# Optimization experiments

Hardware: AMD Instinct MI355X
Metric: run time of the kernel (lower is better)

The kernel has to match this reference:

```python
import jax, jax.numpy as jnp
import numpy as np

DIM, HEAD, SR = 512, 8, 2
LN_EPS = 1e-5


def _layernorm(x, g, b):
    mu = jnp.mean(x, axis=-1, keepdims=True)
    var = jnp.mean((x - mu) ** 2, axis=-1, keepdims=True)
    return (x - mu) * jax.lax.rsqrt(var + LN_EPS) * g + b


def setup_inputs() -> dict:
    key = jax.random.key(0)
    ks = jax.random.split(key, 16)
    B, N, C = 8, 4096, DIM
    s = 1.0 / np.sqrt(C)
    inp = {
        "x": jax.random.normal(ks[0], (B, N, C), jnp.float32),
        "context": jax.random.normal(ks[1], (B, N, C), jnp.float32),
        # Linear weights in torch layout [out, in]
        "Wq": jax.random.normal(ks[2], (C, C), jnp.float32) * s,
        "bq": jnp.zeros((C,), jnp.float32),
        "Wk": jax.random.normal(ks[3], (C, C), jnp.float32) * s,
        "bk": jnp.zeros((C,), jnp.float32),
        "Wv": jax.random.normal(ks[4], (C, C), jnp.float32) * s,
        "bv": jnp.zeros((C,), jnp.float32),
        "Wp": jax.random.normal(ks[5], (C, C), jnp.float32) * s,
        "bp": jnp.zeros((C,), jnp.float32),
        # spatial-reduction convs, OIHW, kernel=stride=SR
        "Wsrk": jax.random.normal(ks[6], (C, C, SR, SR), jnp.float32) * s / SR,
        "bsrk": jnp.zeros((C,), jnp.float32),
        "Wsrv": jax.random.normal(ks[7], (C, C, SR, SR), jnp.float32) * s / SR,
        "bsrv": jnp.zeros((C,), jnp.float32),
        "gk": jnp.ones((C,), jnp.float32),
        "bek": jnp.zeros((C,), jnp.float32),
        "gv": jnp.ones((C,), jnp.float32),
        "bev": jnp.zeros((C,), jnp.float32),
        "H": 64,
        "W": 64,
    }
    return inp


def reference(x, context, Wq, bq, Wk, bk, Wv, bv, Wp, bp,
              Wsrk, bsrk, Wsrv, bsrv, gk, bek, gv, bev, H, W):
    B, N, C = x.shape
    h, d = HEAD, C // HEAD
    scale = d ** (-0.5)

    # spatial reduction on context (sr_ratio > 1 branch)
    ctx = jnp.transpose(context, (0, 2, 1)).reshape(B, C, H, W)  # [B,C,H,W]
    dn = (("NCHW", "OIHW", "NCHW"))

    def sr(kernel, bias):
        y = jax.lax.conv_general_dilated(ctx, kernel, (SR, SR), "VALID",
                                         dimension_numbers=dn)
        y = y + bias[None, :, None, None]
        return jnp.transpose(y.reshape(B, C, -1), (0, 2, 1))  # [B,M,C]

    ctx_k = _layernorm(sr(Wsrk, bsrk), gk, bek)
    ctx_v = _layernorm(sr(Wsrv, bsrv), gv, bev)

    q = (x @ Wq.T + bq).reshape(B, N, h, d)          # [B,N,h,d]
    k = (ctx_k @ Wk.T + bk).reshape(B, -1, h, d)     # [B,M,h,d]
    v = (ctx_v @ Wv.T + bv).reshape(B, -1, h, d)     # [B,M,h,d]

    attn = jnp.einsum("bnhd,bmhd->bhnm", q, k) * scale
    attn = jax.nn.softmax(attn, axis=-1)
    out = jnp.einsum("bhnm,bmhd->bnhd", attn, v).reshape(B, N, C)
    return out @ Wp.T + bp
```

## Files before the change

### kernel.cpp

```cpp
#include <hip/hip_runtime.h>
#include <hip/hip_bf16.h>

typedef float f32x4 __attribute__((ext_vector_type(4)));
typedef short bf16x8 __attribute__((ext_vector_type(8)));
typedef unsigned short ushort_t;

__device__ __forceinline__ ushort_t f2bf(float f) {
    union { float f; unsigned u; } v; v.f = f;
    unsigned r = v.u + 0x7fffu + ((v.u >> 16) & 1u);
    return (ushort_t)(r >> 16);
}
__device__ __forceinline__ float bf2f(ushort_t h) {
    union { unsigned u; float f; } v; v.u = ((unsigned)h) << 16;
    return v.f;
}

__device__ __forceinline__ void async16(ushort_t* lds, const ushort_t* g) {
    __builtin_amdgcn_global_load_lds(
        (const __attribute__((address_space(1))) unsigned int*)g,
        (__attribute__((address_space(3))) unsigned int*)lds, 16, 0, 0);
}

__global__ __launch_bounds__(256) void cast2_bf16_kernel(const float* __restrict__ s0,
                                                         const float* __restrict__ s1,
                                                         ushort_t* __restrict__ dst) {
    long idx = (long)blockIdx.x * 256 + threadIdx.x;
    int sel = (int)(idx >> 21);
    const float* s = sel ? s1 : s0;
    long off = (idx & 2097151) * 8;
    float4 a = *(const float4*)(s + off);
    float4 b = *(const float4*)(s + off + 4);
    ushort_t o[8];
    o[0]=f2bf(a.x); o[1]=f2bf(a.y); o[2]=f2bf(a.z); o[3]=f2bf(a.w);
    o[4]=f2bf(b.x); o[5]=f2bf(b.y); o[6]=f2bf(b.z); o[7]=f2bf(b.w);
    *(bf16x8*)(dst + (long)sel * 16777216 + off) = *(bf16x8*)o;
}

__global__ __launch_bounds__(256) void cast_w4_kernel(const float* __restrict__ s0,
                                                      const float* __restrict__ s1,
                                                      const float* __restrict__ s2,
                                                      const float* __restrict__ s3,
                                                      ushort_t* __restrict__ dst) {
    long idx = (long)blockIdx.x * 256 + threadIdx.x;
    int sel = (int)(idx >> 15);
    const float* s = sel == 0 ? s0 : sel == 1 ? s1 : sel == 2 ? s2 : s3;
    long off = (idx & 32767) * 8;
    float4 a = *(const float4*)(s + off);
    float4 b = *(const float4*)(s + off + 4);
    ushort_t o[8];
    o[0]=f2bf(a.x); o[1]=f2bf(a.y); o[2]=f2bf(a.z); o[3]=f2bf(a.w);
    o[4]=f2bf(b.x); o[5]=f2bf(b.y); o[6]=f2bf(b.z); o[7]=f2bf(b.w);
    *(bf16x8*)(dst + (long)sel * 262144 + off) = *(bf16x8*)o;
}

__global__ __launch_bounds__(256) void pack_wsr2_kernel(const float* __restrict__ w0,
                                                        const float* __restrict__ w1,
                                                        ushort_t* __restrict__ out) {
    int idx = blockIdx.x * 256 + threadIdx.x;
    int sel = idx >> 18;
    const float* w = sel ? w1 : w0;
    int li = idx & 262143;
    int c = li >> 9, ci = li & 511;
    float4 t = *(const float4*)(w + c * 2048 + ci * 4);
    ushort_t* ob = out + sel * 1048576 + c * 2048 + ci;
    ob[0]    = f2bf(t.x);
    ob[512]  = f2bf(t.y);
    ob[1024] = f2bf(t.z);
    ob[1536] = f2bf(t.w);
}

struct GemmJob {
    const ushort_t* A;
    const ushort_t* Bw;
    const float* bias;
    void* C;
    int omode;
    int M;
    int K;
    int gather;
    float oscale;
};

__global__ __launch_bounds__(256) void gemm_multi(GemmJob j0, GemmJob j1, GemmJob j2,
                                                  int nb0, int nb1) {
    __shared__ __align__(16) ushort_t As[128][64];
    __shared__ __align__(16) ushort_t Bs[128][64];
    const int bid = blockIdx.x;
    GemmJob j;
    int local;
    if (bid < nb0)            { j = j0; local = bid; }
    else if (bid < nb0 + nb1) { j = j1; local = bid - nb0; }
    else                      { j = j2; local = bid - nb0 - nb1; }

    const int tid  = threadIdx.x;
    const int row0 = (((local & 7) | ((local >> 5) << 3))) * 128;
    const int col0 = ((local >> 3) & 3) * 128;
    const int wave = tid >> 6, lane = tid & 63;
    const int rw = wave >> 1, cw = wave & 1;
    const int l15 = lane & 15, l4 = lane >> 4;
    const int srow = wave * 8 + (lane >> 3);
    const int sc8  = (lane & 7) * 8;
    const int K = j.K;

    f32x4 acc[4][4] = {};

    for (int k0 = 0; k0 < K; k0 += 64) {
        __syncthreads();
#pragma unroll
        for (int p = 0; p < 4; ++p) {
            int r = p * 32 + srow;
            const ushort_t* ga;
            if (j.gather) {
                int gr = row0 + r;
                int b = gr >> 10, m = gr & 1023;
                int mh = m >> 5, mw = m & 31;
                int tap = k0 >> 9;
                int kh = tap >> 1, kw = tap & 1;
                ga = j.A + ((long)(b * 4096 + (2 * mh + kh) * 64 + (2 * mw + kw))) * 512
                         + (k0 & 511) + sc8;
            } else {
                ga = j.A + (long)(row0 + r) * K + k0 + sc8;
            }
            async16(&As[p * 32 + wave * 8][0], ga);
            async16(&Bs[p * 32 + wave * 8][0],
                    j.Bw + (long)(col0 + r) * K + k0 + sc8);
        }
        __syncthreads();
#pragma unroll
        for (int ks = 0; ks < 2; ++ks) {
            bf16x8 af[4], bfr[4];
#pragma unroll
            for (int i = 0; i < 4; ++i)
                af[i] = *(const bf16x8*)&As[rw * 64 + i * 16 + l15][ks * 32 + l4 * 8];
#pragma unroll
            for (int jj = 0; jj < 4; ++jj)
                bfr[jj] = *(const bf16x8*)&Bs[cw * 64 + jj * 16 + l15][ks * 32 + l4 * 8];
#pragma unroll
            for (int i = 0; i < 4; ++i)
#pragma unroll
                for (int jj = 0; jj < 4; ++jj)
                    acc[i][jj] = __builtin_amdgcn_mfma_f32_16x16x32_bf16(af[i], bfr[jj],
                                                                         acc[i][jj], 0, 0, 0);
        }
    }
#pragma unroll
    for (int i = 0; i < 4; ++i) {
#pragma unroll
        for (int jj = 0; jj < 4; ++jj) {
            int col = col0 + cw * 64 + jj * 16 + l15;
            float bv = j.bias[col];
#pragma unroll
            for (int r = 0; r < 4; ++r) {
                int row = row0 + rw * 64 + i * 16 + l4 * 4 + r;
                float v = (acc[i][jj][r] + bv) * j.oscale;
                if (j.omode == 0) {
                    ((ushort_t*)j.C)[(long)row * 512 + col] = f2bf(v);
                } else if (j.omode == 1) {
                    ((float*)j.C)[(long)row * 512 + col] = v;
                } else {
                    int b = row >> 10, m = row & 1023;
                    int hh = col >> 6, dd = col & 63;
                    ((ushort_t*)j.C)[(((long)(b * 8 + hh) * 64 + dd) << 10) + m] = f2bf(v);
                }
            }
        }
    }
}

__global__ __launch_bounds__(256) void ln_kernel(ushort_t* __restrict__ data,
                                                 const float* __restrict__ g0,
                                                 const float* __restrict__ be0,
                                                 const float* __restrict__ g1,
                                                 const float* __restrict__ be1) {
    int wave = threadIdx.x >> 6, lane = threadIdx.x & 63;
    long row = (long)blockIdx.x * 4 + wave;
    const float* g  = row < 8192 ? g0 : g1;
    const float* be = row < 8192 ? be0 : be1;
    ushort_t* p = data + row * 512 + lane * 8;
    bf16x8 raw = *(bf16x8*)p;
    ushort_t* rp = (ushort_t*)&raw;
    float v[8], s = 0.f, s2 = 0.f;
#pragma unroll
    for (int j = 0; j < 8; ++j) { v[j] = bf2f(rp[j]); s += v[j]; s2 += v[j] * v[j]; }
#pragma unroll
    for (int d = 1; d < 64; d <<= 1) { s += __shfl_xor(s, d); s2 += __shfl_xor(s2, d); }
    float mu  = s * (1.f / 512.f);
    float var = s2 * (1.f / 512.f) - mu * mu;
    float rs  = rsqrtf(var + 1e-5f);
    ushort_t o[8];
#pragma unroll
    for (int j = 0; j < 8; ++j) {
        int c = lane * 8 + j;
        o[j] = f2bf((v[j] - mu) * rs * g[c] + be[c]);
    }
    *(bf16x8*)p = *(bf16x8*)o;
}

__global__ __launch_bounds__(256, 3) void attn_kernel(const ushort_t* __restrict__ q,
                                                      const ushort_t* __restrict__ k,
                                                      const ushort_t* __restrict__ vt,
                                                      ushort_t* __restrict__ o) {
    __shared__ __align__(16) ushort_t Ks[128][72];
    __shared__ __align__(16) ushort_t Vs[64][136];

    const int tid = threadIdx.x;
    const int wave = tid >> 6, lane = tid & 63;
    const int l15 = lane & 15, l4 = lane >> 4;
    const int n0 = blockIdx.x * 128;
    const int hh = blockIdx.y;
    const int b  = blockIdx.z;

    bf16x8 bq[2][2];
#pragma unroll
    for (int nb = 0; nb < 2; ++nb)
#pragma unroll
        for (int ks = 0; ks < 2; ++ks)
            bq[nb][ks] = *(const bf16x8*)(
                q + (long)(b * 4096 + n0 + wave * 32 + nb * 16 + l15) * 512
                  + hh * 64 + ks * 32 + l4 * 8);

    f32x4 oacc[2][4] = {};
    f32x4 lacc[2] = {};
    union { bf16x8 v8; unsigned u[4]; } ones;
    ones.u[0] = ones.u[1] = ones.u[2] = ones.u[3] = 0x3F803F80u;

    for (int c = 0; c < 8; ++c) {
        const int m0 = c * 128;
        __syncthreads();
#pragma unroll
        for (int p = 0; p < 4; ++p) {
            int qi = p * 256 + tid;
            int r = qi >> 3, c8 = (qi & 7) * 8;
            bf16x8 v = *(const bf16x8*)(k + (((long)(b * 1024 + m0 + r) * 8 + hh) << 6) + c8);
            *(bf16x8*)&Ks[r][c8] = v;
        }
#pragma unroll
        for (int p = 0; p < 4; ++p) {
            int qi = p * 256 + tid;
            int dd = qi >> 4, c8 = (qi & 15) * 8;
            bf16x8 v = *(const bf16x8*)(vt + (((long)(b * 8 + hh) * 64 + dd) << 10) + m0 + c8);
            *(bf16x8*)&Vs[dd][c8] = v;
        }
        __syncthreads();

        f32x4 s[2][8] = {};
        __builtin_amdgcn_s_setprio(1);
#pragma unroll
        for (int ks = 0; ks < 2; ++ks) {
#pragma unroll
            for (int i = 0; i < 8; ++i) {
                bf16x8 ak = *(const bf16x8*)&Ks[i * 16 + l15][ks * 32 + l4 * 8];
                s[0][i] = __builtin_amdgcn_mfma_f32_16x16x32_bf16(ak, bq[0][ks], s[0][i], 0, 0, 0);
                s[1][i] = __builtin_amdgcn_mfma_f32_16x16x32_bf16(ak, bq[1][ks], s[1][i], 0, 0, 0);
            }
        }
        __builtin_amdgcn_s_setprio(0);

        unsigned pk[2][8][2];
#pragma unroll
        for (int nb = 0; nb < 2; ++nb)
#pragma unroll
            for (int i = 0; i < 8; ++i) {
                float e0 = __builtin_amdgcn_exp2f(s[nb][i][0]);
                float e1 = __builtin_amdgcn_exp2f(s[nb][i][1]);
                float e2 = __builtin_amdgcn_exp2f(s[nb][i][2]);
                float e3 = __builtin_amdgcn_exp2f(s[nb][i][3]);
                asm("v_cvt_pk_bf16_f32 %0, %1, %2" : "=v"(pk[nb][i][0]) : "v"(e0), "v"(e1));
                asm("v_cvt_pk_bf16_f32 %0, %1, %2" : "=v"(pk[nb][i][1]) : "v"(e2), "v"(e3));
            }

        __builtin_amdgcn_s_setprio(1);
#pragma unroll
        for (int mb = 0; mb < 4; ++mb) {
            union { bf16x8 v8; unsigned long long h[2]; } bfr[4];
#pragma unroll
            for (int db = 0; db < 4; ++db) {
                bfr[db].h[0] = *(const unsigned long long*)&Vs[db * 16 + l15][mb * 32 + l4 * 4];
                bfr[db].h[1] = *(const unsigned long long*)&Vs[db * 16 + l15][mb * 32 + 16 + l4 * 4];
            }
#pragma unroll
            for (int nb = 0; nb < 2; ++nb) {
                union { bf16x8 v8; unsigned u32v[4]; } af;
                af.u32v[0] = pk[nb][2 * mb][0];
                af.u32v[1] = pk[nb][2 * mb][1];
                af.u32v[2] = pk[nb][2 * mb + 1][0];
                af.u32v[3] = pk[nb][2 * mb + 1][1];
                lacc[nb] = __builtin_amdgcn_mfma_f32_16x16x32_bf16(af.v8, ones.v8,
                                                                   lacc[nb], 0, 0, 0);
#pragma unroll
                for (int db = 0; db < 4; ++db)
                    oacc[nb][db] = __builtin_amdgcn_mfma_f32_16x16x32_bf16(af.v8, bfr[db].v8,
                                                                           oacc[nb][db], 0, 0, 0);
            }
        }
        __builtin_amdgcn_s_setprio(0);
    }

#pragma unroll
    for (int nb = 0; nb < 2; ++nb)
#pragma unroll
        for (int r = 0; r < 4; ++r) {
            float inv = 1.f / lacc[nb][r];
            int n = wave * 32 + nb * 16 + l4 * 4 + r;
#pragma unroll
            for (int db = 0; db < 4; ++db) {
                int dd = db * 16 + l15;
                o[((long)(b * 4096 + n0 + n)) * 512 + hh * 64 + dd] = f2bf(oacc[nb][db][r] * inv);
            }
        }
}

extern "C" void kernel_launch(void* const* d_in, const int* in_sizes, int n_in,
                              void* d_out, int out_size, void* d_ws, size_t ws_size,
                              hipStream_t stream) {
    const float* x    = (const float*)d_in[0];
    const float* ctx  = (const float*)d_in[1];
    const float* Wq   = (const float*)d_in[2];
    const float* bq   = (const float*)d_in[3];
    const float* Wk   = (const float*)d_in[4];
    const float* bk   = (const float*)d_in[5];
    const float* Wv   = (const float*)d_in[6];
    const float* bv   = (const float*)d_in[7];
    const float* Wp   = (const float*)d_in[8];
    const float* bp   = (const float*)d_in[9];
    const float* Wsrk = (const float*)d_in[10];
    const float* bsrk = (const float*)d_in[11];
    const float* Wsrv = (const float*)d_in[12];
    const float* bsrv = (const float*)d_in[13];
    const float* gk   = (const float*)d_in[14];
    const float* bek  = (const float*)d_in[15];
    const float* gv   = (const float*)d_in[16];
    const float* bev  = (const float*)d_in[17];

    ushort_t* x_bf    = (ushort_t*)d_ws;
    ushort_t* ctx_bf  = x_bf    + 16777216;
    ushort_t* q_bf    = ctx_bf  + 16777216;
    ushort_t* at_bf   = q_bf    + 16777216;
    ushort_t* k_bf    = at_bf   + 16777216;
    ushort_t* vt_bf   = k_bf    + 4194304;
    ushort_t* convk   = vt_bf   + 4194304;
    ushort_t* convv   = convk   + 4194304;
    ushort_t* wq_bf   = convv   + 4194304;
    ushort_t* wk_bf   = wq_bf   + 262144;
    ushort_t* wv_bf   = wk_bf   + 262144;
    ushort_t* wp_bf   = wv_bf   + 262144;
    ushort_t* wsrk_p  = wp_bf   + 262144;
    ushort_t* wsrv_p  = wsrk_p  + 1048576;

    const float EC = 0.18033688011112042f;

    cast2_bf16_kernel<<<16384, 256, 0, stream>>>(x, ctx, x_bf);
    cast_w4_kernel<<<512, 256, 0, stream>>>(Wq, Wk, Wv, Wp, wq_bf);
    pack_wsr2_kernel<<<2048, 256, 0, stream>>>(Wsrk, Wsrv, wsrk_p);

    GemmJob jck = { ctx_bf, wsrk_p, bsrk, convk, 0, 8192,  2048, 1, 1.0f };
    GemmJob jcv = { ctx_bf, wsrv_p, bsrv, convv, 0, 8192,  2048, 1, 1.0f };
    GemmJob jq  = { x_bf,  wq_bf,  bq,   q_bf,  0, 32768, 512,  0, EC };
    gemm_multi<<<1536, 256, 0, stream>>>(jck, jcv, jq, 256, 256);

    ln_kernel<<<4096, 256, 0, stream>>>(convk, gk, bek, gv, bev);

    GemmJob jk  = { convk, wk_bf, bk, k_bf,  0, 8192, 512, 0, 1.0f };
    GemmJob jv  = { convv, wv_bf, bv, vt_bf, 2, 8192, 512, 0, 1.0f };
    gemm_multi<<<512, 256, 0, stream>>>(jk, jv, jv, 256, 256);

    attn_kernel<<<dim3(32, 8, 8), 256, 0, stream>>>(q_bf, k_bf, vt_bf, at_bf);

    GemmJob jo  = { at_bf, wp_bf, bp, d_out, 1, 32768, 512, 0, 1.0f };
    gemm_multi<<<1024, 256, 0, stream>>>(jo, jo, jo, 1024, 0);
}
```

Before: 435.3 us.

## Fuse fp32-to-bf16 activation cast into GEMM A-tile loads and merge weight prep kernels

Drops the separate cast kernel for x and context. The first GEMM launch now reads fp32 activations directly and converts them to bf16 while staging the A tile into LDS, which removes a full write and re-read of two large bf16 copies. The weight cast and conv-weight pack kernels are also merged into one launch. In exchange, the fp32 A path uses synchronous register loads instead of async global-to-LDS copies. The conv gather now reads each context element four times in fp32 rather than bf16, which doubles the bytes per reread.

```diff
diff --git a/kernel.cpp b/kernel.cpp
--- a/kernel.cpp
+++ b/kernel.cpp
@@ -21,56 +21,43 @@
         (__attribute__((address_space(3))) unsigned int*)lds, 16, 0, 0);
 }
 
-__global__ __launch_bounds__(256) void cast2_bf16_kernel(const float* __restrict__ s0,
-                                                         const float* __restrict__ s1,
-                                                         ushort_t* __restrict__ dst) {
-    long idx = (long)blockIdx.x * 256 + threadIdx.x;
-    int sel = (int)(idx >> 21);
-    const float* s = sel ? s1 : s0;
-    long off = (idx & 2097151) * 8;
-    float4 a = *(const float4*)(s + off);
-    float4 b = *(const float4*)(s + off + 4);
-    ushort_t o[8];
-    o[0]=f2bf(a.x); o[1]=f2bf(a.y); o[2]=f2bf(a.z); o[3]=f2bf(a.w);
-    o[4]=f2bf(b.x); o[5]=f2bf(b.y); o[6]=f2bf(b.z); o[7]=f2bf(b.w);
-    *(bf16x8*)(dst + (long)sel * 16777216 + off) = *(bf16x8*)o;
-}
-
-__global__ __launch_bounds__(256) void cast_w4_kernel(const float* __restrict__ s0,
-                                                      const float* __restrict__ s1,
-                                                      const float* __restrict__ s2,
-                                                      const float* __restrict__ s3,
-                                                      ushort_t* __restrict__ dst) {
-    long idx = (long)blockIdx.x * 256 + threadIdx.x;
-    int sel = (int)(idx >> 15);
-    const float* s = sel == 0 ? s0 : sel == 1 ? s1 : sel == 2 ? s2 : s3;
-    long off = (idx & 32767) * 8;
-    float4 a = *(const float4*)(s + off);
-    float4 b = *(const float4*)(s + off + 4);
-    ushort_t o[8];
-    o[0]=f2bf(a.x); o[1]=f2bf(a.y); o[2]=f2bf(a.z); o[3]=f2bf(a.w);
-    o[4]=f2bf(b.x); o[5]=f2bf(b.y); o[6]=f2bf(b.z); o[7]=f2bf(b.w);
-    *(bf16x8*)(dst + (long)sel * 262144 + off) = *(bf16x8*)o;
-}
-
-__global__ __launch_bounds__(256) void pack_wsr2_kernel(const float* __restrict__ w0,
-                                                        const float* __restrict__ w1,
-                                                        ushort_t* __restrict__ out) {
-    int idx = blockIdx.x * 256 + threadIdx.x;
-    int sel = idx >> 18;
-    const float* w = sel ? w1 : w0;
-    int li = idx & 262143;
-    int c = li >> 9, ci = li & 511;
-    float4 t = *(const float4*)(w + c * 2048 + ci * 4);
-    ushort_t* ob = out + sel * 1048576 + c * 2048 + ci;
-    ob[0]    = f2bf(t.x);
-    ob[512]  = f2bf(t.y);
-    ob[1024] = f2bf(t.z);
-    ob[1536] = f2bf(t.w);
+__global__ __launch_bounds__(256) void prep_w_kernel(const float* __restrict__ Wq,
+                                                     const float* __restrict__ Wk,
+                                                     const float* __restrict__ Wv,
+                                                     const float* __restrict__ Wp,
+                                                     ushort_t* __restrict__ wdst,
+                                                     const float* __restrict__ w0,
+                                                     const float* __restrict__ w1,
+                                                     ushort_t* __restrict__ pout) {
+    int bid = blockIdx.x;
+    if (bid < 512) {
+        long idx = (long)bid * 256 + threadIdx.x;
+        int sel = (int)(idx >> 15);
+        const float* s = sel == 0 ? Wq : sel == 1 ? Wk : sel == 2 ? Wv : Wp;
+        long off = (idx & 32767) * 8;
+        float4 a = *(const float4*)(s + off);
+        float4 b = *(const float4*)(s + off + 4);
+        ushort_t o[8];
+        o[0]=f2bf(a.x); o[1]=f2bf(a.y); o[2]=f2bf(a.z); o[3]=f2bf(a.w);
+        o[4]=f2bf(b.x); o[5]=f2bf(b.y); o[6]=f2bf(b.z); o[7]=f2bf(b.w);
+        *(bf16x8*)(wdst + (long)sel * 262144 + off) = *(bf16x8*)o;
+    } else {
+        int idx = (bid - 512) * 256 + threadIdx.x;
+        int sel = idx >> 18;
+        const float* w = sel ? w1 : w0;
+        int li = idx & 262143;
+        int c = li >> 9, ci = li & 511;
+        float4 t = *(const float4*)(w + c * 2048 + ci * 4);
+        ushort_t* ob = pout + sel * 1048576 + c * 2048 + ci;
+        ob[0]    = f2bf(t.x);
+        ob[512]  = f2bf(t.y);
+        ob[1024] = f2bf(t.z);
+        ob[1536] = f2bf(t.w);
+    }
 }
 
 struct GemmJob {
-    const ushort_t* A;
+    const void* A;
     const ushort_t* Bw;
     const float* bias;
     void* C;
@@ -79,6 +66,7 @@
     int K;
     int gather;
     float oscale;
+    int afp32;
 };
 
 __global__ __launch_bounds__(256) void gemm_multi(GemmJob j0, GemmJob j1, GemmJob j2,
@@ -109,19 +97,29 @@
 #pragma unroll
         for (int p = 0; p < 4; ++p) {
             int r = p * 32 + srow;
-            const ushort_t* ga;
+            long aoff;
             if (j.gather) {
                 int gr = row0 + r;
                 int b = gr >> 10, m = gr & 1023;
                 int mh = m >> 5, mw = m & 31;
                 int tap = k0 >> 9;
                 int kh = tap >> 1, kw = tap & 1;
-                ga = j.A + ((long)(b * 4096 + (2 * mh + kh) * 64 + (2 * mw + kw))) * 512
-                         + (k0 & 511) + sc8;
+                aoff = ((long)(b * 4096 + (2 * mh + kh) * 64 + (2 * mw + kw))) * 512
+                       + (k0 & 511) + sc8;
             } else {
-                ga = j.A + (long)(row0 + r) * K + k0 + sc8;
-            }
-            async16(&As[p * 32 + wave * 8][0], ga);
+                aoff = (long)(row0 + r) * K + k0 + sc8;
+            }
+            if (j.afp32) {
+                const float* ga = (const float*)j.A + aoff;
+                float4 a0 = *(const float4*)ga;
+                float4 a1 = *(const float4*)(ga + 4);
+                ushort_t o[8];
+                o[0]=f2bf(a0.x); o[1]=f2bf(a0.y); o[2]=f2bf(a0.z); o[3]=f2bf(a0.w);
+                o[4]=f2bf(a1.x); o[5]=f2bf(a1.y); o[6]=f2bf(a1.z); o[7]=f2bf(a1.w);
+                *(bf16x8*)&As[r][sc8] = *(bf16x8*)o;
+            } else {
+                async16(&As[p * 32 + wave * 8][0], (const ushort_t*)j.A + aoff);
+            }
             async16(&Bs[p * 32 + wave * 8][0],
                     j.Bw + (long)(col0 + r) * K + k0 + sc8);
         }
@@ -332,9 +330,7 @@
     const float* gv   = (const float*)d_in[16];
     const float* bev  = (const float*)d_in[17];
 
-    ushort_t* x_bf    = (ushort_t*)d_ws;
-    ushort_t* ctx_bf  = x_bf    + 16777216;
-    ushort_t* q_bf    = ctx_bf  + 16777216;
+    ushort_t* q_bf    = (ushort_t*)d_ws + 33554432;
     ushort_t* at_bf   = q_bf    + 16777216;
     ushort_t* k_bf    = at_bf   + 16777216;
     ushort_t* vt_bf   = k_bf    + 4194304;
@@ -349,23 +345,21 @@
 
     const float EC = 0.18033688011112042f;
 
-    cast2_bf16_kernel<<<16384, 256, 0, stream>>>(x, ctx, x_bf);
-    cast_w4_kernel<<<512, 256, 0, stream>>>(Wq, Wk, Wv, Wp, wq_bf);
-    pack_wsr2_kernel<<<2048, 256, 0, stream>>>(Wsrk, Wsrv, wsrk_p);
-
-    GemmJob jck = { ctx_bf, wsrk_p, bsrk, convk, 0, 8192,  2048, 1, 1.0f };
-    GemmJob jcv = { ctx_bf, wsrv_p, bsrv, convv, 0, 8192,  2048, 1, 1.0f };
-    GemmJob jq  = { x_bf,  wq_bf,  bq,   q_bf,  0, 32768, 512,  0, EC };
+    prep_w_kernel<<<2560, 256, 0, stream>>>(Wq, Wk, Wv, Wp, wq_bf, Wsrk, Wsrv, wsrk_p);
+
+    GemmJob jck = { ctx, wsrk_p, bsrk, convk, 0, 8192,  2048, 1, 1.0f, 1 };
+    GemmJob jcv = { ctx, wsrv_p, bsrv, convv, 0, 8192,  2048, 1, 1.0f, 1 };
+    GemmJob jq  = { x,   wq_bf,  bq,   q_bf,  0, 32768, 512,  0, EC,   1 };
     gemm_multi<<<1536, 256, 0, stream>>>(jck, jcv, jq, 256, 256);
 
     ln_kernel<<<4096, 256, 0, stream>>>(convk, gk, bek, gv, bev);
 
-    GemmJob jk  = { convk, wk_bf, bk, k_bf,  0, 8192, 512, 0, 1.0f };
-    GemmJob jv  = { convv, wv_bf, bv, vt_bf, 2, 8192, 512, 0, 1.0f };
+    GemmJob jk  = { convk, wk_bf, bk, k_bf,  0, 8192, 512, 0, 1.0f, 0 };
+    GemmJob jv  = { convv, wv_bf, bv, vt_bf, 2, 8192, 512, 0, 1.0f, 0 };
     gemm_multi<<<512, 256, 0, stream>>>(jk, jv, jv, 256, 256);
 
     attn_kernel<<<dim3(32, 8, 8), 256, 0, stream>>>(q_bf, k_bf, vt_bf, at_bf);
 
-    GemmJob jo  = { at_bf, wp_bf, bp, d_out, 1, 32768, 512, 0, 1.0f };
+    GemmJob jo  = { at_bf, wp_bf, bp, d_out, 1, 32768, 512, 0, 1.0f, 0 };
     gemm_multi<<<1024, 256, 0, stream>>>(jo, jo, jo, 1024, 0);
 }
```

After: 480.5 us. 1.1x slower.
